# Kernel optimization log

Measured on AMD Instinct MI355X. Metric: run time of the kernel, lower is better.

The kernel has to match this reference:

```python
import jax, jax.numpy as jnp
import numpy as np

D_MODEL = 1024
D_K = 64
D_V = 64
N_HEADS = 16
B, S = 2, 2048


def setup_inputs() -> dict:
    key = jax.random.key(0)
    ks = jax.random.split(key, 12)
    scale = 1.0 / np.sqrt(D_MODEL)
    inp = {
        "Q": jax.random.normal(ks[0], (B, S, D_MODEL), jnp.float32),
        "K": jax.random.normal(ks[1], (B, S, D_MODEL), jnp.float32),
        "V": jax.random.normal(ks[2], (B, S, D_MODEL), jnp.float32),
        # per-head projection weights (stacked over heads) and biases
        "Wq": jax.random.normal(ks[3], (N_HEADS, D_MODEL, D_K), jnp.float32) * scale,
        "bq": jax.random.normal(ks[4], (N_HEADS, D_K), jnp.float32) * 0.01,
        "Wk": jax.random.normal(ks[5], (N_HEADS, D_MODEL, D_K), jnp.float32) * scale,
        "bk": jax.random.normal(ks[6], (N_HEADS, D_K), jnp.float32) * 0.01,
        "Wv": jax.random.normal(ks[7], (N_HEADS, D_MODEL, D_V), jnp.float32) * scale,
        "bv": jax.random.normal(ks[8], (N_HEADS, D_V), jnp.float32) * 0.01,
        # output projection: (n_heads*d_v) -> d_model
        "Wo": jax.random.normal(ks[9], (N_HEADS * D_V, D_MODEL), jnp.float32) / np.sqrt(N_HEADS * D_V),
        "bo": jax.random.normal(ks[10], (D_MODEL,), jnp.float32) * 0.01,
    }
    return inp


def reference(Q, K, V, Wq, bq, Wk, bk, Wv, bv, Wo, bo):
    # Per-head projections, vectorized over heads: [B,H,S,dk]
    QW = jnp.einsum("bsd,hdk->bhsk", Q, Wq) + bq[None, :, None, :]
    KW = jnp.einsum("bsd,hdk->bhsk", K, Wk) + bk[None, :, None, :]
    VW = jnp.einsum("bsd,hdv->bhsv", V, Wv) + bv[None, :, None, :]
    # scores: [B,H,S,S]
    scores = jnp.einsum("bhsk,bhtk->bhst", QW, KW)
    # Faithful to torch source: softmax FIRST, then divide by d_k, then by 2
    attn = jax.nn.softmax(scores, axis=-1) / D_K / 2.0
    ctx = jnp.einsum("bhst,bhtv->bhsv", attn, VW)  # [B,H,S,dv]
    # concat heads along last dim (head order == torch concat order)
    ctx = jnp.transpose(ctx, (0, 2, 1, 3)).reshape(B, S, N_HEADS * D_V)
    return ctx @ Wo + bo
```

## Files before the change

### kernel.cpp

```cpp
#include <hip/hip_runtime.h>

typedef unsigned short u16;
typedef unsigned int u32;
typedef __attribute__((ext_vector_type(8))) short bf16x8;
typedef __attribute__((ext_vector_type(4))) float f32x4;

__device__ __forceinline__ u16 f2b(float f) {
    union { float f; u32 u; } v; v.f = f;
    return (u16)((v.u + 0x7FFF + ((v.u >> 16) & 1)) >> 16);
}

__device__ __forceinline__ void glds16(const u16* g, u16* l) {
    __builtin_amdgcn_global_load_lds(
        (const __attribute__((address_space(1))) void*)g,
        (__attribute__((address_space(3))) void*)l, 16, 0, 0);
}

__global__ __launch_bounds__(256) void cast3(
    const float* __restrict__ Q, const float* __restrict__ K,
    const float* __restrict__ V,
    u16* __restrict__ Qb, u16* __restrict__ Kb, u16* __restrict__ Vb)
{
    const float* in = (blockIdx.z == 0) ? Q : (blockIdx.z == 1) ? K : V;
    u16* out = (blockIdx.z == 0) ? Qb : (blockIdx.z == 1) ? Kb : Vb;
    const int n4 = 1048576;
    const int stride = gridDim.x * 256;
    for (int i = blockIdx.x * 256 + threadIdx.x; i < n4; i += stride) {
        float4 v = ((const float4*)in)[i];
        ushort4 o;
        o.x = f2b(v.x); o.y = f2b(v.y); o.z = f2b(v.z); o.w = f2b(v.w);
        ((ushort4*)out)[i] = o;
    }
}

__global__ __launch_bounds__(256) void tcastW(
    const float* __restrict__ Wq, const float* __restrict__ Wk,
    const float* __restrict__ Wv,
    u16* __restrict__ WqT, u16* __restrict__ WkT, u16* __restrict__ WvT)
{
    __shared__ float t[64][68];
    const int sel = blockIdx.z >> 4, hz = blockIdx.z & 15;
    const float* in = (sel == 0) ? Wq : (sel == 1) ? Wk : Wv;
    u16* out = (sel == 0) ? WqT : (sel == 1) ? WkT : WvT;
    const long mb = (long)hz * 65536;
    const int r0 = blockIdx.x * 64;
    const int tid = threadIdx.x;
    const int rr = tid >> 4, c4 = (tid & 15) * 4;

    #pragma unroll
    for (int p = 0; p < 4; ++p) {
        float4 v = *(const float4*)(in + mb + (long)(r0 + p * 16 + rr) * 64 + c4);
        *(float4*)&t[p * 16 + rr][c4] = v;
    }
    __syncthreads();
    #pragma unroll
    for (int p = 0; p < 4; ++p) {
        const int oc = p * 16 + rr;
        const int r4 = (tid & 15) * 4;
        ushort4 o;
        o.x = f2b(t[r4 + 0][oc]); o.y = f2b(t[r4 + 1][oc]);
        o.z = f2b(t[r4 + 2][oc]); o.w = f2b(t[r4 + 3][oc]);
        *(ushort4*)(out + mb + (long)oc * 1024 + r0 + r4) = o;
    }
}

__global__ __launch_bounds__(256) void tcastWo(
    const float* __restrict__ in, u16* __restrict__ out)
{
    __shared__ float t[64][68];
    const int r0 = blockIdx.x * 64, c0 = blockIdx.y * 64;
    const int tid = threadIdx.x;
    const int rr = tid >> 4, c4 = (tid & 15) * 4;

    #pragma unroll
    for (int p = 0; p < 4; ++p) {
        float4 v = *(const float4*)(in + (long)(r0 + p * 16 + rr) * 1024 + c0 + c4);
        *(float4*)&t[p * 16 + rr][c4] = v;
    }
    __syncthreads();
    #pragma unroll
    for (int p = 0; p < 4; ++p) {
        const int oc = p * 16 + rr;
        const int r4 = (tid & 15) * 4;
        ushort4 o;
        o.x = f2b(t[r4 + 0][oc]); o.y = f2b(t[r4 + 1][oc]);
        o.z = f2b(t[r4 + 2][oc]); o.w = f2b(t[r4 + 3][oc]);
        *(ushort4*)(out + (long)(c0 + oc) * 1024 + r0 + r4) = o;
    }
}

#define GEMM_CORE(A_, BT_)                                                     \
    __shared__ u16 As[128 * 64];                                               \
    __shared__ u16 Bs[128 * 64];                                               \
    const int tid = threadIdx.x, lane = tid & 63, w = tid >> 6;                \
    const int m0 = blockIdx.y * 128, n0 = blockIdx.x * 128;                    \
    const int wm = (w >> 1) * 64, wn = (w & 1) * 64;                           \
    const int fr = lane & 15, quad = lane >> 4;                                \
    f32x4 acc[4][4];                                                           \
    const f32x4 zero = {0.f, 0.f, 0.f, 0.f};                                   \
    _Pragma("unroll")                                                          \
    for (int mi = 0; mi < 4; ++mi)                                             \
        _Pragma("unroll")                                                      \
        for (int ni = 0; ni < 4; ++ni) acc[mi][ni] = zero;                     \
    const int srow = lane >> 3;                                                \
    const int schk = (lane & 7) ^ (srow & 7);       \
    const long ga = (long)(m0 + srow) * 1024 + schk * 8;                       \
    const long gb = (long)(n0 + srow) * 1024 + schk * 8;                       \
    const int f7 = fr & 7;                                                     \
    for (int k0 = 0; k0 < 1024; k0 += 64) {                                    \
        __syncthreads();                                                       \
        _Pragma("unroll")                                                      \
        for (int i2 = 0; i2 < 4; ++i2) {                                       \
            const int i = w * 4 + i2;                                          \
            glds16(A_ + ga + (long)i * 8 * 1024 + k0, &As[i * 512]);           \
            glds16(BT_ + gb + (long)i * 8 * 1024 + k0, &Bs[i * 512]);          \
        }                                                                      \
        __syncthreads();                                                       \
        _Pragma("unroll")                                                      \
        for (int kc = 0; kc < 2; ++kc) {                                       \
            const int pos = ((kc * 4 + quad) ^ f7) * 8;                        \
            bf16x8 af[4], bfr[4];                                              \
            _Pragma("unroll")                                                  \
            for (int mi = 0; mi < 4; ++mi)                                     \
                af[mi] = *(const bf16x8*)&As[(wm + mi * 16 + fr) * 64 + pos];  \
            _Pragma("unroll")                                                  \
            for (int ni = 0; ni < 4; ++ni)                                     \
                bfr[ni] = *(const bf16x8*)&Bs[(wn + ni * 16 + fr) * 64 + pos]; \
            _Pragma("unroll")                                                  \
            for (int mi = 0; mi < 4; ++mi)                                     \
                _Pragma("unroll")                                              \
                for (int ni = 0; ni < 4; ++ni)                                 \
                    acc[mi][ni] = __builtin_amdgcn_mfma_f32_16x16x32_bf16(     \
                        af[mi], bfr[ni], acc[mi][ni], 0, 0, 0);                \
        }                                                                      \
    }

__global__ __launch_bounds__(256) void proj3(
    const u16* __restrict__ Qb, const u16* __restrict__ Kb,
    const u16* __restrict__ Vb,
    const u16* __restrict__ WqT, const u16* __restrict__ WkT,
    const u16* __restrict__ WvT,
    const float* __restrict__ bq, const float* __restrict__ bk,
    const float* __restrict__ bv,
    u16* __restrict__ QWb, u16* __restrict__ KWb, u16* __restrict__ VWb)
{
    const int z = blockIdx.z;
    const u16* A  = (z == 0) ? Qb : (z == 1) ? Kb : Vb;
    const u16* BT = (z == 0) ? WqT : (z == 1) ? WkT : WvT;
    const float* bias = (z == 0) ? bq : (z == 1) ? bk : bv;
    u16* Cu = (z == 0) ? QWb : (z == 1) ? KWb : VWb;

    GEMM_CORE(A, BT)

    #pragma unroll
    for (int mi = 0; mi < 4; ++mi) {
        #pragma unroll
        for (int ni = 0; ni < 4; ++ni) {
            #pragma unroll
            for (int r = 0; r < 4; ++r) {
                const int m = m0 + wm + mi * 16 + quad * 4 + r;
                const int c = n0 + wn + ni * 16 + fr;
                const float v = acc[mi][ni][r] + bias[c];
                const int b = m >> 11, s = m & 2047, h = c >> 6, k = c & 63;
                if (z != 2)
                    Cu[((long)(b * 16 + h) * 2048 + s) * 64 + k] = f2b(v);
                else
                    Cu[((long)(b * 16 + h) * 64 + k) * 2048 + s] = f2b(v);
            }
        }
    }
}

__global__ __launch_bounds__(256) void gemm_out(
    const u16* __restrict__ A, const u16* __restrict__ BT,
    const float* __restrict__ bias, float* __restrict__ Cf)
{
    GEMM_CORE(A, BT)

    #pragma unroll
    for (int mi = 0; mi < 4; ++mi) {
        #pragma unroll
        for (int ni = 0; ni < 4; ++ni) {
            #pragma unroll
            for (int r = 0; r < 4; ++r) {
                const int m = m0 + wm + mi * 16 + quad * 4 + r;
                const int c = n0 + wn + ni * 16 + fr;
                Cf[(long)m * 1024 + c] = acc[mi][ni][r] + bias[c];
            }
        }
    }
}

__global__ __launch_bounds__(256) void attn_mfma(
    const u16* __restrict__ QW, const u16* __restrict__ KW,
    const u16* __restrict__ VW, u16* __restrict__ ctxb)
{
    __shared__ u16 kt[2][64 * 64];
    __shared__ u16 vt[2][64 * 64];
    __shared__ u16 ps[4][32 * 72];

    const int tid = threadIdx.x, lane = tid & 63, w = tid >> 6;
    const int bh = blockIdx.y, b = bh >> 4, h = bh & 15;
    const int q0 = blockIdx.x * 128;
    const int fr = lane & 15, quad = lane >> 4;
    const int f7 = fr & 7;

    bf16x8 aQ[2][2];
    #pragma unroll
    for (int s = 0; s < 2; ++s) {
        const u16* qp = QW + ((long)bh * 2048 + q0 + w * 32 + s * 16 + fr) * 64;
        aQ[s][0] = *(const bf16x8*)(qp + quad * 8);
        aQ[s][1] = *(const bf16x8*)(qp + 32 + quad * 8);
    }

    const f32x4 zero = {0.f, 0.f, 0.f, 0.f};
    f32x4 acc[2][4], lac[2];
    #pragma unroll
    for (int s = 0; s < 2; ++s) {
        lac[s] = zero;
        #pragma unroll
        for (int d = 0; d < 4; ++d) acc[s][d] = zero;
    }
    bf16x8 bones;
    #pragma unroll
    for (int j = 0; j < 8; ++j) bones[j] = (short)0x3F80;

    const int srow = lane >> 3;
    const int schk = (lane & 7) ^ (srow & 7);
    const long kgb = (long)bh * (2048 * 64);
    const long vgb = (long)bh * (64 * 2048);

#define ATTN_STAGE(p_, t_)                                                    \
    _Pragma("unroll")                                                         \
    for (int i2 = 0; i2 < 2; ++i2) {                                          \
        const int i = w * 2 + i2;                                             \
        glds16(KW + kgb + (long)((t_) + i * 8 + srow) * 64 + schk * 8,        \
               &kt[p_][i * 512]);                                             \
        glds16(VW + vgb + (long)(i * 8 + srow) * 2048 + (t_) + schk * 8,      \
               &vt[p_][i * 512]);                                             \
    }

    ATTN_STAGE(0, 0)
    __syncthreads();

    const int pos0 = (quad ^ f7) * 8;
    const int pos1 = pos0 ^ 32;
    u16* pw = ps[w];

    for (int t0 = 0; t0 < 2048; t0 += 64) {
        const int p = (t0 >> 6) & 1;
        if (t0 + 64 < 2048) { ATTN_STAGE(p ^ 1, t0 + 64) }

        const u16* ktp = kt[p];
        const u16* vtp = vt[p];

        f32x4 sc[2][4];
        __builtin_amdgcn_s_setprio(1);
        #pragma unroll
        for (int s = 0; s < 2; ++s) {
            #pragma unroll
            for (int sub = 0; sub < 4; ++sub) {
                const int row = (sub * 16 + fr) * 64;
                bf16x8 k0 = *(const bf16x8*)&ktp[row + pos0];
                bf16x8 k1 = *(const bf16x8*)&ktp[row + pos1];
                f32x4 z = __builtin_amdgcn_mfma_f32_16x16x32_bf16(k0, aQ[s][0], zero, 0, 0, 0);
                sc[s][sub] = __builtin_amdgcn_mfma_f32_16x16x32_bf16(k1, aQ[s][1], z, 0, 0, 0);
            }
        }
        __builtin_amdgcn_s_setprio(0);

        #pragma unroll
        for (int s = 0; s < 2; ++s) {
            #pragma unroll
            for (int sub = 0; sub < 4; ++sub) {
                float e0 = __expf(sc[s][sub][0]);
                float e1 = __expf(sc[s][sub][1]);
                float e2 = __expf(sc[s][sub][2]);
                float e3 = __expf(sc[s][sub][3]);
                u32 lo, hi;
                asm("v_cvt_pk_bf16_f32 %0, %1, %2" : "=v"(lo) : "v"(e0), "v"(e1));
                asm("v_cvt_pk_bf16_f32 %0, %1, %2" : "=v"(hi) : "v"(e2), "v"(e3));
                uint2 pk2; pk2.x = lo; pk2.y = hi;
                *(uint2*)&pw[(s * 16 + fr) * 72 + sub * 16 + quad * 4] = pk2;
            }
        }
        __asm__ volatile("s_waitcnt lgkmcnt(0)" ::: "memory");

        __builtin_amdgcn_s_setprio(1);
        #pragma unroll
        for (int s = 0; s < 2; ++s) {
            const bf16x8 aP0 = *(const bf16x8*)&pw[(s * 16 + fr) * 72 + quad * 8];
            const bf16x8 aP1 = *(const bf16x8*)&pw[(s * 16 + fr) * 72 + 32 + quad * 8];
            lac[s] = __builtin_amdgcn_mfma_f32_16x16x32_bf16(aP0, bones, lac[s], 0, 0, 0);
            lac[s] = __builtin_amdgcn_mfma_f32_16x16x32_bf16(aP1, bones, lac[s], 0, 0, 0);
            #pragma unroll
            for (int d = 0; d < 4; ++d) {
                const int row = (d * 16 + fr) * 64;
                bf16x8 v0 = *(const bf16x8*)&vtp[row + pos0];
                bf16x8 v1 = *(const bf16x8*)&vtp[row + pos1];
                acc[s][d] = __builtin_amdgcn_mfma_f32_16x16x32_bf16(aP0, v0, acc[s][d], 0, 0, 0);
                acc[s][d] = __builtin_amdgcn_mfma_f32_16x16x32_bf16(aP1, v1, acc[s][d], 0, 0, 0);
            }
        }
        __builtin_amdgcn_s_setprio(0);
        __syncthreads();
    }

    #pragma unroll
    for (int s = 0; s < 2; ++s) {
        #pragma unroll
        for (int r = 0; r < 4; ++r) {
            const float scl = 1.0f / (lac[s][r] * 128.0f);
            const long row = (long)b * 2048 + q0 + w * 32 + s * 16 + quad * 4 + r;
            #pragma unroll
            for (int d = 0; d < 4; ++d)
                ctxb[row * 1024 + h * 64 + d * 16 + fr] = f2b(acc[s][d][r] * scl);
        }
    }
}

extern "C" void kernel_launch(void* const* d_in, const int* in_sizes, int n_in,
                              void* d_out, int out_size, void* d_ws, size_t ws_size,
                              hipStream_t stream) {
    (void)in_sizes; (void)n_in; (void)out_size; (void)ws_size;

    const float* Q  = (const float*)d_in[0];
    const float* K  = (const float*)d_in[1];
    const float* V  = (const float*)d_in[2];
    const float* Wq = (const float*)d_in[3];
    const float* bq = (const float*)d_in[4];
    const float* Wk = (const float*)d_in[5];
    const float* bk = (const float*)d_in[6];
    const float* Wv = (const float*)d_in[7];
    const float* bv = (const float*)d_in[8];
    const float* Wo = (const float*)d_in[9];
    const float* bo = (const float*)d_in[10];
    float* out = (float*)d_out;

    u16* ws  = (u16*)d_ws;
    u16* Qb  = ws;
    u16* Kb  = Qb  + 4194304;
    u16* Vb  = Kb  + 4194304;
    u16* WqT = Vb  + 4194304;
    u16* WkT = WqT + 1048576;
    u16* WvT = WkT + 1048576;
    u16* WoT = WvT + 1048576;
    u16* QWb = WoT + 1048576;
    u16* KWb = QWb + 4194304;
    u16* VWb = KWb + 4194304;
    u16* ctx = VWb + 4194304;

    cast3<<<dim3(1024, 1, 3), 256, 0, stream>>>(Q, K, V, Qb, Kb, Vb);
    tcastW<<<dim3(16, 1, 48), 256, 0, stream>>>(Wq, Wk, Wv, WqT, WkT, WvT);
    tcastWo<<<dim3(16, 16), 256, 0, stream>>>(Wo, WoT);

    proj3<<<dim3(8, 32, 3), 256, 0, stream>>>(Qb, Kb, Vb, WqT, WkT, WvT,
                                              bq, bk, bv, QWb, KWb, VWb);

    attn_mfma<<<dim3(16, 32), 256, 0, stream>>>(QWb, KWb, VWb, ctx);

    gemm_out<<<dim3(8, 32), 256, 0, stream>>>(ctx, WoT, bo, out);
}
```

Before: 250.2 us.

## Double-buffer GEMM LDS tiles, swap block raster order, vectorize V-transposed stores

The shared GEMM core now uses two LDS buffers and prefetches the next k-tile through global_load_lds while computing the current one, raising wave priority around the MFMA block. The previous loop waited on a barrier after every load. The grid mapping is swapped so consecutive blocks walk along M instead of N, which changes L2 reuse of the weight tiles. The projection epilogue hoists the bias load and writes the transposed V output as ushort4 vectors. Doubling LDS to 64KB per block may reduce occupancy.

```diff
diff --git a/kernel.cpp b/kernel.cpp
--- a/kernel.cpp
+++ b/kernel.cpp
@@ -89,11 +89,19 @@
     }
 }
 
+#define GEMM_STAGE(A_, BT_, p_, k_)                                            \
+    _Pragma("unroll")                                                          \
+    for (int i2 = 0; i2 < 4; ++i2) {                                           \
+        const int i = w * 4 + i2;                                              \
+        glds16(A_ + ga + (long)i * 8 * 1024 + (k_), &As[p_][i * 512]);         \
+        glds16(BT_ + gb + (long)i * 8 * 1024 + (k_), &Bs[p_][i * 512]);        \
+    }
+
 #define GEMM_CORE(A_, BT_)                                                     \
-    __shared__ u16 As[128 * 64];                                               \
-    __shared__ u16 Bs[128 * 64];                                               \
+    __shared__ u16 As[2][128 * 64];                                            \
+    __shared__ u16 Bs[2][128 * 64];                                            \
     const int tid = threadIdx.x, lane = tid & 63, w = tid >> 6;                \
-    const int m0 = blockIdx.y * 128, n0 = blockIdx.x * 128;                    \
+    const int m0 = blockIdx.x * 128, n0 = blockIdx.y * 128;                    \
     const int wm = (w >> 1) * 64, wn = (w & 1) * 64;                           \
     const int fr = lane & 15, quad = lane >> 4;                                \
     f32x4 acc[4][4];                                                           \
@@ -107,25 +115,22 @@
     const long ga = (long)(m0 + srow) * 1024 + schk * 8;                       \
     const long gb = (long)(n0 + srow) * 1024 + schk * 8;                       \
     const int f7 = fr & 7;                                                     \
+    GEMM_STAGE(A_, BT_, 0, 0)                                                  \
+    __syncthreads();                                                           \
     for (int k0 = 0; k0 < 1024; k0 += 64) {                                    \
-        __syncthreads();                                                       \
-        _Pragma("unroll")                                                      \
-        for (int i2 = 0; i2 < 4; ++i2) {                                       \
-            const int i = w * 4 + i2;                                          \
-            glds16(A_ + ga + (long)i * 8 * 1024 + k0, &As[i * 512]);           \
-            glds16(BT_ + gb + (long)i * 8 * 1024 + k0, &Bs[i * 512]);          \
-        }                                                                      \
-        __syncthreads();                                                       \
+        const int p = (k0 >> 6) & 1;                                           \
+        if (k0 + 64 < 1024) { GEMM_STAGE(A_, BT_, p ^ 1, k0 + 64) }            \
+        __builtin_amdgcn_s_setprio(1);                                         \
         _Pragma("unroll")                                                      \
         for (int kc = 0; kc < 2; ++kc) {                                       \
             const int pos = ((kc * 4 + quad) ^ f7) * 8;                        \
             bf16x8 af[4], bfr[4];                                              \
             _Pragma("unroll")                                                  \
             for (int mi = 0; mi < 4; ++mi)                                     \
-                af[mi] = *(const bf16x8*)&As[(wm + mi * 16 + fr) * 64 + pos];  \
+                af[mi] = *(const bf16x8*)&As[p][(wm + mi * 16 + fr) * 64 + pos]; \
             _Pragma("unroll")                                                  \
             for (int ni = 0; ni < 4; ++ni)                                     \
-                bfr[ni] = *(const bf16x8*)&Bs[(wn + ni * 16 + fr) * 64 + pos]; \
+                bfr[ni] = *(const bf16x8*)&Bs[p][(wn + ni * 16 + fr) * 64 + pos]; \
             _Pragma("unroll")                                                  \
             for (int mi = 0; mi < 4; ++mi)                                     \
                 _Pragma("unroll")                                              \
@@ -133,6 +138,8 @@
                     acc[mi][ni] = __builtin_amdgcn_mfma_f32_16x16x32_bf16(     \
                         af[mi], bfr[ni], acc[mi][ni], 0, 0, 0);                \
         }                                                                      \
+        __builtin_amdgcn_s_setprio(0);                                         \
+        __syncthreads();                                                       \
     }
 
 __global__ __launch_bounds__(256) void proj3(
@@ -156,16 +163,22 @@
     for (int mi = 0; mi < 4; ++mi) {
         #pragma unroll
         for (int ni = 0; ni < 4; ++ni) {
-            #pragma unroll
-            for (int r = 0; r < 4; ++r) {
-                const int m = m0 + wm + mi * 16 + quad * 4 + r;
-                const int c = n0 + wn + ni * 16 + fr;
-                const float v = acc[mi][ni][r] + bias[c];
-                const int b = m >> 11, s = m & 2047, h = c >> 6, k = c & 63;
-                if (z != 2)
-                    Cu[((long)(b * 16 + h) * 2048 + s) * 64 + k] = f2b(v);
-                else
-                    Cu[((long)(b * 16 + h) * 64 + k) * 2048 + s] = f2b(v);
+            const int mB = m0 + wm + mi * 16 + quad * 4;
+            const int c  = n0 + wn + ni * 16 + fr;
+            const int b = mB >> 11, s = mB & 2047, h = c >> 6, k = c & 63;
+            const float bi = bias[c];
+            if (z != 2) {
+                #pragma unroll
+                for (int r = 0; r < 4; ++r)
+                    Cu[((long)(b * 16 + h) * 2048 + s + r) * 64 + k] =
+                        f2b(acc[mi][ni][r] + bi);
+            } else {
+                ushort4 o;
+                o.x = f2b(acc[mi][ni][0] + bi);
+                o.y = f2b(acc[mi][ni][1] + bi);
+                o.z = f2b(acc[mi][ni][2] + bi);
+                o.w = f2b(acc[mi][ni][3] + bi);
+                *(ushort4*)&Cu[((long)(b * 16 + h) * 64 + k) * 2048 + s] = o;
             }
         }
     }
@@ -354,10 +367,10 @@
     tcastW<<<dim3(16, 1, 48), 256, 0, stream>>>(Wq, Wk, Wv, WqT, WkT, WvT);
     tcastWo<<<dim3(16, 16), 256, 0, stream>>>(Wo, WoT);
 
-    proj3<<<dim3(8, 32, 3), 256, 0, stream>>>(Qb, Kb, Vb, WqT, WkT, WvT,
+    proj3<<<dim3(32, 8, 3), 256, 0, stream>>>(Qb, Kb, Vb, WqT, WkT, WvT,
                                               bq, bk, bv, QWb, KWb, VWb);
 
     attn_mfma<<<dim3(16, 32), 256, 0, stream>>>(QWb, KWb, VWb, ctx);
 
-    gemm_out<<<dim3(8, 32), 256, 0, stream>>>(ctx, WoT, bo, out);
-}
+    gemm_out<<<dim3(32, 8), 256, 0, stream>>>(ctx, WoT, bo, out);
+}
```

New measurement: 230.0 us. -8.1%, faster.
